# Kernel tuning notes

Measured on AMD Instinct MI355X. Metric: run time of the kernel, lower is better.

The kernel has to match this reference:

```python
import jax, jax.numpy as jnp
import numpy as np

N_NODES = 50000
N_EDGES = 800000
N_GRAPHS = 64
IN_C = 64
HID = 64
HEADS = 4
NEG_SLOPE = 0.2
EPS = 1e-16


def setup_inputs() -> dict:
    key = jax.random.key(0)
    ks = jax.random.split(key, 16)
    x = jax.random.normal(ks[0], (N_NODES, IN_C), dtype=jnp.float32)
    edge_index = jax.random.randint(ks[1], (2, N_EDGES), 0, N_NODES, dtype=jnp.int64)
    batch = jnp.sort(jax.random.randint(ks[2], (N_NODES,), 0, N_GRAPHS, dtype=jnp.int64))
    s = 1.0 / np.sqrt(IN_C)
    s2 = 1.0 / np.sqrt(HID * HEADS)
    s3 = 1.0 / np.sqrt(HID)
    return {
        "x": x,
        "edge_index": edge_index,
        "batch": batch,
        # GATv2 layer 1: in 64 -> heads*64 = 256 (concat)
        "Wl1": jax.random.normal(ks[3], (IN_C, HEADS * HID), dtype=jnp.float32) * s,
        "Wr1": jax.random.normal(ks[4], (IN_C, HEADS * HID), dtype=jnp.float32) * s,
        "att1": jax.random.normal(ks[5], (HEADS, HID), dtype=jnp.float32) * s3,
        "b1": jnp.zeros((HEADS * HID,), dtype=jnp.float32),
        # GATv2 layer 2: in 256 -> 1 head * 64
        "Wl2": jax.random.normal(ks[6], (HEADS * HID, HID), dtype=jnp.float32) * s2,
        "Wr2": jax.random.normal(ks[7], (HEADS * HID, HID), dtype=jnp.float32) * s2,
        "att2": jax.random.normal(ks[8], (1, HID), dtype=jnp.float32) * s3,
        "b2": jnp.zeros((HID,), dtype=jnp.float32),
        # MLP head: 64 -> 64 -> 2
        "W3": jax.random.normal(ks[9], (HID, 64), dtype=jnp.float32) * s3,
        "b3": jnp.zeros((64,), dtype=jnp.float32),
        "W4": jax.random.normal(ks[10], (64, 2), dtype=jnp.float32) * (1.0 / 8.0),
        "b4": jnp.zeros((2,), dtype=jnp.float32),
    }


def gatv2_conv(x, src, dst, Wl, Wr, att, bias, heads, out_c, n_nodes):
    # PyG GATv2Conv (eval mode, add_self_loops=False, concat heads):
    # x_l = lin_l(x) used for SOURCE nodes (messages), x_r = lin_r(x) for TARGET nodes.
    xl = (x @ Wl).reshape(n_nodes, heads, out_c)
    xr = (x @ Wr).reshape(n_nodes, heads, out_c)
    e = jax.nn.leaky_relu(xl[src] + xr[dst], NEG_SLOPE)          # [E, H, C]
    logits = jnp.einsum('ehc,hc->eh', e, att)                    # [E, H]
    # numerically stable softmax over incoming edges of each target node
    m = jax.ops.segment_max(logits, dst, num_segments=n_nodes)   # [N, H]
    ex = jnp.exp(logits - m[dst])
    denom = jax.ops.segment_sum(ex, dst, num_segments=n_nodes)   # [N, H]
    alpha = ex / (denom[dst] + EPS)                              # [E, H]
    out = jax.ops.segment_sum(alpha[:, :, None] * xl[src], dst, num_segments=n_nodes)
    return out.reshape(n_nodes, heads * out_c) + bias


def reference(x, edge_index, batch, Wl1, Wr1, att1, b1, Wl2, Wr2, att2, b2, W3, b3, W4, b4):
    src, dst = edge_index[0], edge_index[1]
    n = x.shape[0]
    h = gatv2_conv(x, src, dst, Wl1, Wr1, att1, b1, HEADS, HID, n)
    h = jax.nn.elu(h)
    h = gatv2_conv(h, src, dst, Wl2, Wr2, att2, b2, 1, HID, n)
    h = jax.nn.elu(h)
    # global mean pool over graphs
    sums = jax.ops.segment_sum(h, batch, num_segments=N_GRAPHS)
    cnt = jax.ops.segment_sum(jnp.ones((n,), dtype=h.dtype), batch, num_segments=N_GRAPHS)
    pooled = sums / jnp.maximum(cnt, 1.0)[:, None]
    # MLP head (dropout inactive in eval)
    z = jax.nn.relu(pooled @ W3 + b3)
    return z @ W4 + b4
```

## Files before the change

kernel.cpp:

```cpp
#include <hip/hip_runtime.h>
#include <hip/hip_fp16.h>
#include <math.h>

#define N_NODES 50000
#define N_EDGES 800000
#define N_GRAPHS 64
#define L2E 1.44269504f

#if __has_builtin(__builtin_amdgcn_fdot2)
#define HAS_FDOT2 1
typedef _Float16 h2_t __attribute__((ext_vector_type(2)));
#else
#define HAS_FDOT2 0
#endif

typedef _Float16 f16x8 __attribute__((ext_vector_type(8)));
typedef float f32x4 __attribute__((ext_vector_type(4)));

__device__ __forceinline__ float elu1(float v){ return v > 0.f ? v : expm1f(v); }

__device__ __forceinline__ float pkdot(float4 q, const __half2* r2,
        const __half2* A6, const __half2* A4){
    const __half2* qh = (const __half2*)&q;
    float p = 0.f;
#if HAS_FDOT2
    #pragma unroll
    for (int i=0;i<4;i++){
        __half2 u = __hadd2(qh[i], r2[i]);
        __half2 ua = __builtin_bit_cast(__half2,
            __builtin_bit_cast(unsigned, u) & 0x7FFF7FFFu);
        p = __builtin_amdgcn_fdot2(__builtin_bit_cast(h2_t,u),
                                   __builtin_bit_cast(h2_t,A6[i]), p, false);
        p = __builtin_amdgcn_fdot2(__builtin_bit_cast(h2_t,ua),
                                   __builtin_bit_cast(h2_t,A4[i]), p, false);
    }
#else
    #pragma unroll
    for (int i=0;i<4;i++){
        float2 qf = __half22float2(qh[i]);
        float2 rf = __half22float2(r2[i]);
        float2 s6 = __half22float2(A6[i]);
        float2 s4 = __half22float2(A4[i]);
        float u0 = qf.x + rf.x, u1 = qf.y + rf.y;
        p = fmaf(s6.x, u0, fmaf(s4.x, fabsf(u0), p));
        p = fmaf(s6.y, u1, fmaf(s4.y, fabsf(u1), p));
    }
#endif
    return p;
}

__global__ __launch_bounds__(256) void k_prep(const float* __restrict__ x,
        const float* __restrict__ Wl1, const float* __restrict__ Wr1,
        const float* __restrict__ Wl2, const float* __restrict__ Wr2,
        const int* __restrict__ ei,
        __half* __restrict__ xh, __half* __restrict__ Wt1, __half* __restrict__ Wt2,
        int* __restrict__ deg, int* __restrict__ ranks, float* __restrict__ pooled){
    int t = threadIdx.x, bk = blockIdx.x;
    if (bk < 3125){
        int idx = bk*256 + t;
        float4 v = ((const float4*)x)[idx];
        __half2* dst = (__half2*)xh + (size_t)idx*2;
        dst[0] = __floats2half2_rn(v.x, v.y);
        dst[1] = __floats2half2_rn(v.z, v.w);
    } else if (bk < 3381){
        int elem = (bk-3125)*256 + t;
        if (elem < 32768){
            int c = elem >> 6, k = elem & 63;
            float v = (c < 256) ? Wl1[k*256 + c] : Wr1[k*256 + (c-256)];
            Wt1[elem] = __float2half(v);
        } else {
            int e2 = elem - 32768;
            int c = e2 >> 8, k = e2 & 255;
            float v = (c < 64) ? Wl2[k*64 + c] : Wr2[k*64 + (c-64)];
            Wt2[e2] = __float2half(v);
        }
        if (elem < N_GRAPHS*64) pooled[elem] = 0.f;
    } else {
        int e4 = (bk-3381)*256 + t;
        if (e4 < N_EDGES/4){
            int4 d = ((const int4*)(ei + N_EDGES))[e4];
            int4 r;
            r.x = atomicAdd(&deg[d.x],1);
            r.y = atomicAdd(&deg[d.y],1);
            r.z = atomicAdd(&deg[d.z],1);
            r.w = atomicAdd(&deg[d.w],1);
            ((int4*)ranks)[e4] = r;
        }
    }
}

__global__ __launch_bounds__(1024) void k_scan_a(const int* __restrict__ deg,
        int* __restrict__ rowptr, int* __restrict__ partial){
    __shared__ int s[1024];
    int t = threadIdx.x; int i = blockIdx.x*1024 + t;
    int v = (i < N_NODES) ? deg[i] : 0;
    s[t] = v; __syncthreads();
    for (int off=1; off<1024; off<<=1){
        int add = (t>=off) ? s[t-off] : 0;
        __syncthreads();
        s[t] += add;
        __syncthreads();
    }
    if (i < N_NODES) rowptr[i] = s[t] - v;
    if (t == 1023) partial[blockIdx.x] = s[1023];
}

__global__ __launch_bounds__(1024) void k_scan_c(int* __restrict__ rowptr,
        const int* __restrict__ partial){
    __shared__ int base;
    if (threadIdx.x == 0){
        int run = 0;
        for (int bk=0; bk<(int)blockIdx.x; bk++) run += partial[bk];
        base = run;
    }
    __syncthreads();
    int i = blockIdx.x*1024 + threadIdx.x;
    if (i < N_NODES){
        rowptr[i] += base;
    } else if (i == N_NODES){
        rowptr[N_NODES] = N_EDGES;
    }
}

__global__ __launch_bounds__(256) void k_mm1(const __half* __restrict__ xh,
        const __half* __restrict__ Wt1,
        __half* __restrict__ xl1h, __half* __restrict__ xr1h,
        const int* __restrict__ ei, const int* __restrict__ ranks,
        const int* __restrict__ rowptr, int* __restrict__ srcs){
    if (blockIdx.y == 4){
        int e4 = blockIdx.x*256 + threadIdx.x;
        if (e4 < N_EDGES/4){
            int4 sv = ((const int4*)ei)[e4];
            int4 dv = ((const int4*)(ei + N_EDGES))[e4];
            int4 rv = ((const int4*)ranks)[e4];
            __builtin_nontemporal_store(sv.x, &srcs[rowptr[dv.x] + rv.x]);
            __builtin_nontemporal_store(sv.y, &srcs[rowptr[dv.y] + rv.y]);
            __builtin_nontemporal_store(sv.z, &srcs[rowptr[dv.z] + rv.z]);
            __builtin_nontemporal_store(sv.w, &srcs[rowptr[dv.w] + rv.w]);
        }
        return;
    }
    __shared__ __half lds[4][16*136];
    int w = threadIdx.x >> 6, l = threadIdx.x & 63;
    int r0 = blockIdx.x*64 + w*16;
    int cg = blockIdx.y;
    int lr = l & 15, lk = l >> 4, lk4 = lk*4;
    int ar = r0 + lr; if (ar >= N_NODES) ar = N_NODES-1;
    const __half* arow = xh + (size_t)ar*64;
    f16x8 a0 = *(const f16x8*)(arow + lk*8);
    f16x8 a1 = *(const f16x8*)(arow + 32 + lk*8);
    f32x4 acc[8];
    #pragma unroll
    for (int ct=0; ct<8; ct++) acc[ct] = (f32x4){0.f,0.f,0.f,0.f};
    #pragma unroll
    for (int ct=0; ct<8; ct++){
        int col = cg*128 + ct*16 + lr;
        const __half* brow = Wt1 + (size_t)col*64;
        f16x8 b0 = *(const f16x8*)(brow + lk*8);
        f16x8 b1 = *(const f16x8*)(brow + 32 + lk*8);
        acc[ct] = __builtin_amdgcn_mfma_f32_16x16x32_f16(a0, b0, acc[ct], 0,0,0);
        acc[ct] = __builtin_amdgcn_mfma_f32_16x16x32_f16(a1, b1, acc[ct], 0,0,0);
    }
    #pragma unroll
    for (int ct=0; ct<8; ct++){
        #pragma unroll
        for (int i=0;i<4;i++)
            lds[w][(lk4+i)*136 + ct*16 + lr] = __float2half(acc[ct][i]);
    }
    __half* base = (cg < 2) ? xl1h : xr1h;
    int cbase = (cg & 1)*128;
    #pragma unroll
    for (int rr=0; rr<4; rr++){
        int row = rr*4 + lk;
        float4 v = *(const float4*)&lds[w][row*136 + lr*8];
        int grow = r0 + row;
        if (grow < N_NODES)
            *(float4*)&base[(size_t)grow*256 + cbase + lr*8] = v;
    }
}

__global__ __launch_bounds__(256) void k_mm2(const __half* __restrict__ h1h,
        const __half* __restrict__ Wt2,
        __half* __restrict__ xl2h, __half* __restrict__ xr2h){
    __shared__ __half lds[4][16*72];
    int w = threadIdx.x >> 6, l = threadIdx.x & 63;
    int r0 = blockIdx.x*64 + w*16;
    int cg = blockIdx.y;
    int lr = l & 15, lk = l >> 4, lk4 = lk*4;
    int ar = r0 + lr; if (ar >= N_NODES) ar = N_NODES-1;
    const __half* arow = h1h + (size_t)ar*256;
    f32x4 acc[4];
    #pragma unroll
    for (int ct=0; ct<4; ct++) acc[ct] = (f32x4){0.f,0.f,0.f,0.f};
    #pragma unroll
    for (int ks=0; ks<8; ks++){
        f16x8 a = *(const f16x8*)(arow + ks*32 + lk*8);
        #pragma unroll
        for (int ct=0; ct<4; ct++){
            int col = cg*64 + ct*16 + lr;
            f16x8 bf = *(const f16x8*)(Wt2 + (size_t)col*256 + ks*32 + lk*8);
            acc[ct] = __builtin_amdgcn_mfma_f32_16x16x32_f16(a, bf, acc[ct], 0,0,0);
        }
    }
    #pragma unroll
    for (int ct=0; ct<4; ct++){
        #pragma unroll
        for (int i=0;i<4;i++)
            lds[w][(lk4+i)*72 + ct*16 + lr] = __float2half(acc[ct][i]);
    }
    __half* base = (cg == 0) ? xl2h : xr2h;
    #pragma unroll
    for (int rr=0; rr<2; rr++){
        int row = rr*8 + (l>>3);
        float4 v = *(const float4*)&lds[w][row*72 + (l&7)*8];
        int grow = r0 + row;
        if (grow < N_NODES)
            *(float4*)&base[(size_t)grow*64 + (l&7)*8] = v;
    }
}

__global__ __launch_bounds__(256) void k_gat1(const __half* __restrict__ xlh,
        const __half* __restrict__ xrh, const int* __restrict__ srcs,
        const int* __restrict__ rowptr, const float* __restrict__ att,
        const float* __restrict__ b, __half* __restrict__ h1h){
    int w = threadIdx.x >> 6, l = threadIdx.x & 63;
    int n = blockIdx.x*4 + w;
    int g = l >> 5, sub = l & 31;
    const float4* xh4 = (const float4*)xlh;
    float4 rq = *(const float4*)(xrh + (size_t)n*256 + sub*8);
    __half2 r2[4];
    { const __half2* rh = (const __half2*)&rq;
      r2[0]=rh[0]; r2[1]=rh[1]; r2[2]=rh[2]; r2[3]=rh[3]; }
    float4 A0v = *(const float4*)(att + sub*8);
    float4 A1v = *(const float4*)(att + sub*8 + 4);
    const float C6 = 0.6f*L2E, C4 = 0.4f*L2E;
    __half2 A6[4] = { __floats2half2_rn(A0v.x*C6, A0v.y*C6),
                      __floats2half2_rn(A0v.z*C6, A0v.w*C6),
                      __floats2half2_rn(A1v.x*C6, A1v.y*C6),
                      __floats2half2_rn(A1v.z*C6, A1v.w*C6) };
    __half2 A4[4] = { __floats2half2_rn(A0v.x*C4, A0v.y*C4),
                      __floats2half2_rn(A0v.z*C4, A0v.w*C4),
                      __floats2half2_rn(A1v.x*C4, A1v.y*C4),
                      __floats2half2_rn(A1v.z*C4, A1v.w*C4) };
    const __half2 Z2 = __floats2half2_rn(0.f, 0.f);
    float accf[8];
    #pragma unroll
    for (int c=0;c<8;c++) accf[c]=0.f;
    float dacc = 0.f;
    int beg = rowptr[n], end = rowptr[n+1];

    auto body = [&](int j, bool checked){
        int j0=j+g, j1=j+2+g, j2=j+4+g, j3=j+6+g;
        bool c0=true, c1=true, c2=true, c3=true;
        if (checked){
            c0 = j0<end; c1 = j1<end; c2 = j2<end; c3 = j3<end;
            j0 = c0?j0:beg; j1 = c1?j1:beg; j2 = c2?j2:beg; j3 = c3?j3:beg;
        }
        int s0 = srcs[j0], s1 = srcs[j1], s2 = srcs[j2], s3 = srcs[j3];
        float4 q0 = xh4[(size_t)(unsigned)s0*32 + sub];
        float4 q1 = xh4[(size_t)(unsigned)s1*32 + sub];
        float4 q2 = xh4[(size_t)(unsigned)s2*32 + sub];
        float4 q3 = xh4[(size_t)(unsigned)s3*32 + sub];
        float p0 = pkdot(q0, r2, A6, A4);
        float p1 = pkdot(q1, r2, A6, A4);
        float p2 = pkdot(q2, r2, A6, A4);
        float p3 = pkdot(q3, r2, A6, A4);
        #pragma unroll
        for (int off=1; off<8; off<<=1){
            p0 += __shfl_xor(p0, off);
            p1 += __shfl_xor(p1, off);
            p2 += __shfl_xor(p2, off);
            p3 += __shfl_xor(p3, off);
        }
        float e0 = exp2f(p0), e1 = exp2f(p1), e2 = exp2f(p2), e3 = exp2f(p3);
        if (checked){
            e0 = c0?e0:0.f; e1 = c1?e1:0.f; e2 = c2?e2:0.f; e3 = c3?e3:0.f;
        }
        __half2 E0 = __half2half2(__float2half_rn(e0));
        __half2 E1 = __half2half2(__float2half_rn(e1));
        __half2 E2 = __half2half2(__float2half_rn(e2));
        __half2 E3 = __half2half2(__float2half_rn(e3));
        const __half2* q0h = (const __half2*)&q0;
        const __half2* q1h = (const __half2*)&q1;
        const __half2* q2h = (const __half2*)&q2;
        const __half2* q3h = (const __half2*)&q3;
        #pragma unroll
        for (int i=0;i<4;i++){
            __half2 a16 = __hfma2(E0, q0h[i], Z2);
            a16 = __hfma2(E1, q1h[i], a16);
            a16 = __hfma2(E2, q2h[i], a16);
            a16 = __hfma2(E3, q3h[i], a16);
            float2 f = __half22float2(a16);
            accf[2*i]   += f.x;
            accf[2*i+1] += f.y;
        }
        dacc += e0 + e1 + e2 + e3;
    };

    int j = beg;
    int nfull = (end - beg) >> 3;
    for (int it=0; it<nfull; ++it, j+=8) body(j, false);
    if (j < end) body(j, true);

    #pragma unroll
    for (int c=0;c<8;c++) accf[c] += __shfl_xor(accf[c], 32);
    dacc += __shfl_xor(dacc, 32);
    if (l < 32){
        float inv = 1.f / (dacc + 1e-16f);
        float4 B0 = *(const float4*)(b + l*8);
        float4 B1 = *(const float4*)(b + l*8 + 4);
        float4 st;
        __half2* sp = (__half2*)&st;
        sp[0] = __floats2half2_rn(elu1(fmaf(accf[0],inv,B0.x)), elu1(fmaf(accf[1],inv,B0.y)));
        sp[1] = __floats2half2_rn(elu1(fmaf(accf[2],inv,B0.z)), elu1(fmaf(accf[3],inv,B0.w)));
        sp[2] = __floats2half2_rn(elu1(fmaf(accf[4],inv,B1.x)), elu1(fmaf(accf[5],inv,B1.y)));
        sp[3] = __floats2half2_rn(elu1(fmaf(accf[6],inv,B1.z)), elu1(fmaf(accf[7],inv,B1.w)));
        *(float4*)(h1h + (size_t)n*256 + l*8) = st;
    }
}

__global__ __launch_bounds__(256) void k_gat2(const __half* __restrict__ xlh,
        const __half* __restrict__ xrh, const int* __restrict__ srcs,
        const int* __restrict__ rowptr, const float* __restrict__ att,
        const float* __restrict__ b, float* __restrict__ h2){
    int w = threadIdx.x >> 6, l = threadIdx.x & 63;
    int n = blockIdx.x*4 + w;
    int g = l >> 3, sub = l & 7;
    const float4* xh4 = (const float4*)xlh;
    float4 rq = *(const float4*)(xrh + (size_t)n*64 + sub*8);
    __half2 r2[4];
    { const __half2* rh = (const __half2*)&rq;
      r2[0]=rh[0]; r2[1]=rh[1]; r2[2]=rh[2]; r2[3]=rh[3]; }
    float4 A0v = *(const float4*)(att + sub*8);
    float4 A1v = *(const float4*)(att + sub*8 + 4);
    const float C6 = 0.6f*L2E, C4 = 0.4f*L2E;
    __half2 A6[4] = { __floats2half2_rn(A0v.x*C6, A0v.y*C6),
                      __floats2half2_rn(A0v.z*C6, A0v.w*C6),
                      __floats2half2_rn(A1v.x*C6, A1v.y*C6),
                      __floats2half2_rn(A1v.z*C6, A1v.w*C6) };
    __half2 A4[4] = { __floats2half2_rn(A0v.x*C4, A0v.y*C4),
                      __floats2half2_rn(A0v.z*C4, A0v.w*C4),
                      __floats2half2_rn(A1v.x*C4, A1v.y*C4),
                      __floats2half2_rn(A1v.z*C4, A1v.w*C4) };
    const __half2 Z2 = __floats2half2_rn(0.f, 0.f);
    __half2 a16[4] = {Z2, Z2, Z2, Z2};
    float dacc = 0.f;
    int beg = rowptr[n], end = rowptr[n+1];

    auto body = [&](int j, bool checked){
        int j0 = j+g, j1 = j+8+g;
        bool c0=true, c1=true;
        if (checked){
            c0 = j0<end; c1 = j1<end;
            j0 = c0?j0:beg; j1 = c1?j1:beg;
        }
        int s0 = srcs[j0], s1 = srcs[j1];
        float4 q0 = xh4[(size_t)(unsigned)s0*8 + sub];
        float4 q1 = xh4[(size_t)(unsigned)s1*8 + sub];
        float p0 = pkdot(q0, r2, A6, A4);
        float p1 = pkdot(q1, r2, A6, A4);
        #pragma unroll
        for (int off=1; off<8; off<<=1){
            p0 += __shfl_xor(p0, off);
            p1 += __shfl_xor(p1, off);
        }
        float e0 = exp2f(p0), e1 = exp2f(p1);
        if (checked){ e0 = c0?e0:0.f; e1 = c1?e1:0.f; }
        __half2 E0 = __half2half2(__float2half_rn(e0));
        __half2 E1 = __half2half2(__float2half_rn(e1));
        const __half2* q0h = (const __half2*)&q0;
        const __half2* q1h = (const __half2*)&q1;
        #pragma unroll
        for (int i=0;i<4;i++){
            a16[i] = __hfma2(E0, q0h[i], a16[i]);
            a16[i] = __hfma2(E1, q1h[i], a16[i]);
        }
        dacc += e0 + e1;
    };

    int j = beg;
    int nfull = (end - beg) >> 4;
    for (int it=0; it<nfull; ++it, j+=16) body(j, false);
    if (j < end) body(j, true);

    float accf[8];
    #pragma unroll
    for (int i=0;i<4;i++){
        float2 f = __half22float2(a16[i]);
        accf[2*i] = f.x; accf[2*i+1] = f.y;
    }
    #pragma unroll
    for (int off=8; off<64; off<<=1){
        #pragma unroll
        for (int c=0;c<8;c++) accf[c] += __shfl_xor(accf[c], off);
        dacc += __shfl_xor(dacc, off);
    }
    if (l < 8){
        float inv = 1.f / (dacc + 1e-16f);
        float4 B0 = *(const float4*)(b + l*8);
        float4 B1 = *(const float4*)(b + l*8 + 4);
        float4 o0, o1;
        o0.x = elu1(fmaf(accf[0], inv, B0.x));
        o0.y = elu1(fmaf(accf[1], inv, B0.y));
        o0.z = elu1(fmaf(accf[2], inv, B0.z));
        o0.w = elu1(fmaf(accf[3], inv, B0.w));
        o1.x = elu1(fmaf(accf[4], inv, B1.x));
        o1.y = elu1(fmaf(accf[5], inv, B1.y));
        o1.z = elu1(fmaf(accf[6], inv, B1.z));
        o1.w = elu1(fmaf(accf[7], inv, B1.w));
        float4* op = (float4*)(h2 + (size_t)n*64 + l*8);
        op[0] = o0; op[1] = o1;
    }
}

__device__ __forceinline__ int lower_bound_i(const int* a, int n, int key){
    int lo = 0, hi = n;
    while (lo < hi){ int mid = (lo+hi)>>1; if (a[mid] < key) lo = mid+1; else hi = mid; }
    return lo;
}

__global__ __launch_bounds__(256) void k_pool(const float* __restrict__ h2,
        const int* __restrict__ batch, float* __restrict__ pooled){
    int gph = blockIdx.x, part = blockIdx.y;
    int t = threadIdx.x, c = t & 63, q = t >> 6;
    int start = lower_bound_i(batch, N_NODES, gph);
    int end   = lower_bound_i(batch, N_NODES, gph+1);
    int len = end - start;
    int is = start + (int)(((long long)len*part) >> 3);
    int ie = start + (int)(((long long)len*(part+1)) >> 3);
    float s = 0.f;
    for (int i = is + q; i < ie; i += 4) s += h2[(size_t)i*64 + c];
    __shared__ float red[256];
    red[t] = s; __syncthreads();
    if (q == 0){
        float tot = red[c] + red[64+c] + red[128+c] + red[192+c];
        atomicAdd(&pooled[gph*64 + c], tot);
    }
}

__global__ __launch_bounds__(64) void k_mlp(const float* __restrict__ pooled,
        const int* __restrict__ batch,
        const float* __restrict__ W3, const float* __restrict__ b3,
        const float* __restrict__ W4, const float* __restrict__ b4,
        float* __restrict__ out){
    int gph = blockIdx.x, t = threadIdx.x;
    __shared__ float ps[64], zs[64];
    int start = lower_bound_i(batch, N_NODES, gph);
    int end   = lower_bound_i(batch, N_NODES, gph+1);
    float cnt = fmaxf((float)(end - start), 1.f);
    ps[t] = pooled[gph*64 + t] / cnt;
    __syncthreads();
    float a = b3[t];
    for (int k=0;k<64;k++) a = fmaf(ps[k], W3[k*64+t], a);
    zs[t] = fmaxf(a, 0.f); __syncthreads();
    if (t < 2){
        float o = b4[t];
        for (int k=0;k<64;k++) o = fmaf(zs[k], W4[k*2+t], o);
        out[gph*2 + t] = o;
    }
}

extern "C" void kernel_launch(void* const* d_in, const int* in_sizes, int n_in,
                              void* d_out, int out_size, void* d_ws, size_t ws_size,
                              hipStream_t stream) {
    const float* x    = (const float*)d_in[0];
    const int*   ei   = (const int*)  d_in[1];
    const int*   batch= (const int*)  d_in[2];
    const float* Wl1  = (const float*)d_in[3];
    const float* Wr1  = (const float*)d_in[4];
    const float* att1 = (const float*)d_in[5];
    const float* b1   = (const float*)d_in[6];
    const float* Wl2  = (const float*)d_in[7];
    const float* Wr2  = (const float*)d_in[8];
    const float* att2 = (const float*)d_in[9];
    const float* b2   = (const float*)d_in[10];
    const float* W3   = (const float*)d_in[11];
    const float* b3   = (const float*)d_in[12];
    const float* W4   = (const float*)d_in[13];
    const float* b4   = (const float*)d_in[14];
    float* out = (float*)d_out;

    char* wsp = (char*)d_ws;
    size_t off = 0;
    auto alloc = [&](size_t bytes) -> char* {
        char* p = wsp + off; off += (bytes + 255) & ~(size_t)255; return p;
    };
    __half* xh    = (__half*)alloc((size_t)N_NODES*64*2);
    __half* Wt1   = (__half*)alloc(512*64*2);
    __half* Wt2   = (__half*)alloc(128*256*2);
    __half* xl1h  = (__half*)alloc((size_t)N_NODES*256*2);
    __half* xr1h  = (__half*)alloc((size_t)N_NODES*256*2);
    __half* h1h   = (__half*)alloc((size_t)N_NODES*256*2);
    int* rowptr   = (int*)alloc((N_NODES+1)*4);
    int* partial  = (int*)alloc(64*4);
    int* srcs     = (int*)alloc((size_t)N_EDGES*4);
    int* ranks    = (int*)alloc((size_t)N_EDGES*4);
    int* deg      = (int*)alloc(N_NODES*4);
    float* pooled = (float*)alloc(N_GRAPHS*64*4);
    __half* xl2h  = xl1h;
    __half* xr2h  = xl1h + (size_t)N_NODES*64;
    float*  h2    = (float*)xr1h;

    hipMemsetAsync(deg, 0, (size_t)N_NODES*sizeof(int), stream);
    k_prep<<<3125+256+782, 256, 0, stream>>>(x, Wl1, Wr1, Wl2, Wr2, ei,
                                             xh, Wt1, Wt2, deg, ranks, pooled);
    k_scan_a<<<49, 1024, 0, stream>>>(deg, rowptr, partial);
    k_scan_c<<<49, 1024, 0, stream>>>(rowptr, partial);

    k_mm1<<<dim3(782,5), 256, 0, stream>>>(xh, Wt1, xl1h, xr1h,
                                           ei, ranks, rowptr, srcs);
    k_gat1<<<N_NODES/4, 256, 0, stream>>>(xl1h, xr1h, srcs, rowptr, att1, b1, h1h);
    k_mm2<<<dim3(782,2), 256, 0, stream>>>(h1h, Wt2, xl2h, xr2h);
    k_gat2<<<N_NODES/4, 256, 0, stream>>>(xl2h, xr2h, srcs, rowptr, att2, b2, h2);
    k_pool<<<dim3(N_GRAPHS,8), 256, 0, stream>>>(h2, batch, pooled);
    k_mlp<<<N_GRAPHS, 64, 0, stream>>>(pooled, batch, W3, b3, W4, b4, out);
}
```

Baseline: 257.2 us.

## Merge scan into single-block kernel and loop column groups inside matmul blocks

Replaces the two-kernel, 49-block prefix scan with a single-block scan in which each thread serially sums 49 degrees, removing one launch. The mm1 and mm2 kernels now loop over column groups inside each block instead of spreading them across grid.y, so the A-row fragments are loaded once and reused. The gather index math in the GAT kernels uses 32-bit unsigned arithmetic instead of size_t. This trades grid parallelism for fewer blocks and launches, and the single-block scan makes strided, uncoalesced reads.

```diff
diff --git a/kernel.cpp b/kernel.cpp
--- a/kernel.cpp
+++ b/kernel.cpp
@@ -89,37 +89,34 @@
     }
 }
 
-__global__ __launch_bounds__(1024) void k_scan_a(const int* __restrict__ deg,
-        int* __restrict__ rowptr, int* __restrict__ partial){
+__global__ __launch_bounds__(1024) void k_scan(const int* __restrict__ deg,
+        int* __restrict__ rowptr){
     __shared__ int s[1024];
-    int t = threadIdx.x; int i = blockIdx.x*1024 + t;
-    int v = (i < N_NODES) ? deg[i] : 0;
-    s[t] = v; __syncthreads();
+    const int PER = 49;
+    int t = threadIdx.x;
+    int base = t*PER;
+    int sum = 0;
+    for (int i=0;i<PER;i++){
+        int idx = base+i;
+        if (idx < N_NODES) sum += deg[idx];
+    }
+    s[t] = sum; __syncthreads();
     for (int off=1; off<1024; off<<=1){
         int add = (t>=off) ? s[t-off] : 0;
         __syncthreads();
         s[t] += add;
         __syncthreads();
     }
-    if (i < N_NODES) rowptr[i] = s[t] - v;
-    if (t == 1023) partial[blockIdx.x] = s[1023];
-}
-
-__global__ __launch_bounds__(1024) void k_scan_c(int* __restrict__ rowptr,
-        const int* __restrict__ partial){
-    __shared__ int base;
-    if (threadIdx.x == 0){
-        int run = 0;
-        for (int bk=0; bk<(int)blockIdx.x; bk++) run += partial[bk];
-        base = run;
-    }
-    __syncthreads();
-    int i = blockIdx.x*1024 + threadIdx.x;
-    if (i < N_NODES){
-        rowptr[i] += base;
-    } else if (i == N_NODES){
-        rowptr[N_NODES] = N_EDGES;
-    }
+    int run = s[t] - sum;
+    for (int i=0;i<PER;i++){
+        int idx = base+i;
+        if (idx < N_NODES){
+            int d = deg[idx];
+            rowptr[idx] = run;
+            run += d;
+        }
+    }
+    if (t == 1023) rowptr[N_NODES] = N_EDGES;
 }
 
 __global__ __launch_bounds__(256) void k_mm1(const __half* __restrict__ xh,
@@ -127,7 +124,7 @@
         __half* __restrict__ xl1h, __half* __restrict__ xr1h,
         const int* __restrict__ ei, const int* __restrict__ ranks,
         const int* __restrict__ rowptr, int* __restrict__ srcs){
-    if (blockIdx.y == 4){
+    if (blockIdx.y == 1){
         int e4 = blockIdx.x*256 + threadIdx.x;
         if (e4 < N_EDGES/4){
             int4 sv = ((const int4*)ei)[e4];
@@ -143,39 +140,41 @@
     __shared__ __half lds[4][16*136];
     int w = threadIdx.x >> 6, l = threadIdx.x & 63;
     int r0 = blockIdx.x*64 + w*16;
-    int cg = blockIdx.y;
     int lr = l & 15, lk = l >> 4, lk4 = lk*4;
     int ar = r0 + lr; if (ar >= N_NODES) ar = N_NODES-1;
     const __half* arow = xh + (size_t)ar*64;
     f16x8 a0 = *(const f16x8*)(arow + lk*8);
     f16x8 a1 = *(const f16x8*)(arow + 32 + lk*8);
-    f32x4 acc[8];
-    #pragma unroll
-    for (int ct=0; ct<8; ct++) acc[ct] = (f32x4){0.f,0.f,0.f,0.f};
-    #pragma unroll
-    for (int ct=0; ct<8; ct++){
-        int col = cg*128 + ct*16 + lr;
-        const __half* brow = Wt1 + (size_t)col*64;
-        f16x8 b0 = *(const f16x8*)(brow + lk*8);
-        f16x8 b1 = *(const f16x8*)(brow + 32 + lk*8);
-        acc[ct] = __builtin_amdgcn_mfma_f32_16x16x32_f16(a0, b0, acc[ct], 0,0,0);
-        acc[ct] = __builtin_amdgcn_mfma_f32_16x16x32_f16(a1, b1, acc[ct], 0,0,0);
-    }
-    #pragma unroll
-    for (int ct=0; ct<8; ct++){
-        #pragma unroll
-        for (int i=0;i<4;i++)
-            lds[w][(lk4+i)*136 + ct*16 + lr] = __float2half(acc[ct][i]);
-    }
-    __half* base = (cg < 2) ? xl1h : xr1h;
-    int cbase = (cg & 1)*128;
-    #pragma unroll
-    for (int rr=0; rr<4; rr++){
-        int row = rr*4 + lk;
-        float4 v = *(const float4*)&lds[w][row*136 + lr*8];
-        int grow = r0 + row;
-        if (grow < N_NODES)
-            *(float4*)&base[(size_t)grow*256 + cbase + lr*8] = v;
+    #pragma unroll
+    for (int cg=0; cg<4; cg++){
+        f32x4 acc[8];
+        #pragma unroll
+        for (int ct=0; ct<8; ct++) acc[ct] = (f32x4){0.f,0.f,0.f,0.f};
+        #pragma unroll
+        for (int ct=0; ct<8; ct++){
+            int col = cg*128 + ct*16 + lr;
+            const __half* brow = Wt1 + (size_t)col*64;
+            f16x8 b0 = *(const f16x8*)(brow + lk*8);
+            f16x8 b1 = *(const f16x8*)(brow + 32 + lk*8);
+            acc[ct] = __builtin_amdgcn_mfma_f32_16x16x32_f16(a0, b0, acc[ct], 0,0,0);
+            acc[ct] = __builtin_amdgcn_mfma_f32_16x16x32_f16(a1, b1, acc[ct], 0,0,0);
+        }
+        #pragma unroll
+        for (int ct=0; ct<8; ct++){
+            #pragma unroll
+            for (int i=0;i<4;i++)
+                lds[w][(lk4+i)*136 + ct*16 + lr] = __float2half(acc[ct][i]);
+        }
+        __half* base = (cg < 2) ? xl1h : xr1h;
+        int cbase = (cg & 1)*128;
+        #pragma unroll
+        for (int rr=0; rr<4; rr++){
+            int row = rr*4 + lk;
+            float4 v = *(const float4*)&lds[w][row*136 + lr*8];
+            int grow = r0 + row;
+            if (grow < N_NODES)
+                *(float4*)&base[(size_t)grow*256 + cbase + lr*8] = v;
+        }
     }
 }
 
@@ -185,37 +184,41 @@
     __shared__ __half lds[4][16*72];
     int w = threadIdx.x >> 6, l = threadIdx.x & 63;
     int r0 = blockIdx.x*64 + w*16;
-    int cg = blockIdx.y;
     int lr = l & 15, lk = l >> 4, lk4 = lk*4;
     int ar = r0 + lr; if (ar >= N_NODES) ar = N_NODES-1;
     const __half* arow = h1h + (size_t)ar*256;
-    f32x4 acc[4];
-    #pragma unroll
-    for (int ct=0; ct<4; ct++) acc[ct] = (f32x4){0.f,0.f,0.f,0.f};
-    #pragma unroll
-    for (int ks=0; ks<8; ks++){
-        f16x8 a = *(const f16x8*)(arow + ks*32 + lk*8);
+    f16x8 a[8];
+    #pragma unroll
+    for (int ks=0; ks<8; ks++) a[ks] = *(const f16x8*)(arow + ks*32 + lk*8);
+    #pragma unroll
+    for (int cg=0; cg<2; cg++){
+        f32x4 acc[4];
+        #pragma unroll
+        for (int ct=0; ct<4; ct++) acc[ct] = (f32x4){0.f,0.f,0.f,0.f};
+        #pragma unroll
+        for (int ks=0; ks<8; ks++){
+            #pragma unroll
+            for (int ct=0; ct<4; ct++){
+                int col = cg*64 + ct*16 + lr;
+                f16x8 bf = *(const f16x8*)(Wt2 + (size_t)col*256 + ks*32 + lk*8);
+                acc[ct] = __builtin_amdgcn_mfma_f32_16x16x32_f16(a[ks], bf, acc[ct], 0,0,0);
+            }
+        }
         #pragma unroll
         for (int ct=0; ct<4; ct++){
-            int col = cg*64 + ct*16 + lr;
-            f16x8 bf = *(const f16x8*)(Wt2 + (size_t)col*256 + ks*32 + lk*8);
-            acc[ct] = __builtin_amdgcn_mfma_f32_16x16x32_f16(a, bf, acc[ct], 0,0,0);
-        }
-    }
-    #pragma unroll
-    for (int ct=0; ct<4; ct++){
-        #pragma unroll
-        for (int i=0;i<4;i++)
-            lds[w][(lk4+i)*72 + ct*16 + lr] = __float2half(acc[ct][i]);
-    }
-    __half* base = (cg == 0) ? xl2h : xr2h;
-    #pragma unroll
-    for (int rr=0; rr<2; rr++){
-        int row = rr*8 + (l>>3);
-        float4 v = *(const float4*)&lds[w][row*72 + (l&7)*8];
-        int grow = r0 + row;
-        if (grow < N_NODES)
-            *(float4*)&base[(size_t)grow*64 + (l&7)*8] = v;
+            #pragma unroll
+            for (int i=0;i<4;i++)
+                lds[w][(lk4+i)*72 + ct*16 + lr] = __float2half(acc[ct][i]);
+        }
+        __half* base = (cg == 0) ? xl2h : xr2h;
+        #pragma unroll
+        for (int rr=0; rr<2; rr++){
+            int row = rr*8 + (l>>3);
+            float4 v = *(const float4*)&lds[w][row*72 + (l&7)*8];
+            int grow = r0 + row;
+            if (grow < N_NODES)
+                *(float4*)&base[(size_t)grow*64 + (l&7)*8] = v;
+        }
     }
 }
 
@@ -257,10 +260,10 @@
             j0 = c0?j0:beg; j1 = c1?j1:beg; j2 = c2?j2:beg; j3 = c3?j3:beg;
         }
         int s0 = srcs[j0], s1 = srcs[j1], s2 = srcs[j2], s3 = srcs[j3];
-        float4 q0 = xh4[(size_t)(unsigned)s0*32 + sub];
-        float4 q1 = xh4[(size_t)(unsigned)s1*32 + sub];
-        float4 q2 = xh4[(size_t)(unsigned)s2*32 + sub];
-        float4 q3 = xh4[(size_t)(unsigned)s3*32 + sub];
+        float4 q0 = xh4[(unsigned)(s0*32 + sub)];
+        float4 q1 = xh4[(unsigned)(s1*32 + sub)];
+        float4 q2 = xh4[(unsigned)(s2*32 + sub)];
+        float4 q3 = xh4[(unsigned)(s3*32 + sub)];
         float p0 = pkdot(q0, r2, A6, A4);
         float p1 = pkdot(q1, r2, A6, A4);
         float p2 = pkdot(q2, r2, A6, A4);
@@ -355,8 +358,8 @@
             j0 = c0?j0:beg; j1 = c1?j1:beg;
         }
         int s0 = srcs[j0], s1 = srcs[j1];
-        float4 q0 = xh4[(size_t)(unsigned)s0*8 + sub];
-        float4 q1 = xh4[(size_t)(unsigned)s1*8 + sub];
+        float4 q0 = xh4[(unsigned)(s0*8 + sub)];
+        float4 q1 = xh4[(unsigned)(s1*8 + sub)];
         float p0 = pkdot(q0, r2, A6, A4);
         float p1 = pkdot(q1, r2, A6, A4);
         #pragma unroll
@@ -492,7 +495,6 @@
     __half* xr1h  = (__half*)alloc((size_t)N_NODES*256*2);
     __half* h1h   = (__half*)alloc((size_t)N_NODES*256*2);
     int* rowptr   = (int*)alloc((N_NODES+1)*4);
-    int* partial  = (int*)alloc(64*4);
     int* srcs     = (int*)alloc((size_t)N_EDGES*4);
     int* ranks    = (int*)alloc((size_t)N_EDGES*4);
     int* deg      = (int*)alloc(N_NODES*4);
@@ -504,13 +506,12 @@
     hipMemsetAsync(deg, 0, (size_t)N_NODES*sizeof(int), stream);
     k_prep<<<3125+256+782, 256, 0, stream>>>(x, Wl1, Wr1, Wl2, Wr2, ei,
                                              xh, Wt1, Wt2, deg, ranks, pooled);
-    k_scan_a<<<49, 1024, 0, stream>>>(deg, rowptr, partial);
-    k_scan_c<<<49, 1024, 0, stream>>>(rowptr, partial);
-
-    k_mm1<<<dim3(782,5), 256, 0, stream>>>(xh, Wt1, xl1h, xr1h,
+    k_scan<<<1, 1024, 0, stream>>>(deg, rowptr);
+
+    k_mm1<<<dim3(782,2), 256, 0, stream>>>(xh, Wt1, xl1h, xr1h,
                                            ei, ranks, rowptr, srcs);
     k_gat1<<<N_NODES/4, 256, 0, stream>>>(xl1h, xr1h, srcs, rowptr, att1, b1, h1h);
-    k_mm2<<<dim3(782,2), 256, 0, stream>>>(h1h, Wt2, xl2h, xr2h);
+    k_mm2<<<782, 256, 0, stream>>>(h1h, Wt2, xl2h, xr2h);
     k_gat2<<<N_NODES/4, 256, 0, stream>>>(xl2h, xr2h, srcs, rowptr, att2, b2, h2);
     k_pool<<<dim3(N_GRAPHS,8), 256, 0, stream>>>(h2, batch, pooled);
     k_mlp<<<N_GRAPHS, 64, 0, stream>>>(pooled, batch, W3, b3, W4, b4, out);
```

New measurement: 344.7 us. 34.0% more time.
